# Kernel tuning notes

Measured on AMD Instinct MI355X. Metric: run time of the kernel, lower is better.

## Reference

```python
import jax, jax.numpy as jnp
import numpy as np

B, T, C, H = 2, 2048, 1024, 4
D = C // H
STRIDES = [1, 3, 7, 13]  # spiral_strides[:n_head]
SCALE = 1.0 / float(np.sqrt(D))


def _build_mask():
    """Static [H, T, T] bool mask: spiral positions intersected with causal.
    Replicates: positions = set((i+offset)%T for offset in range(-T//2, T//2, stride)),
    then keep only p <= i."""
    m = np.zeros((H, T, T), dtype=bool)
    i = np.arange(T)
    causal = (np.arange(T)[None, :] <= i[:, None])
    for h in range(H):
        s = STRIDES[h % len(STRIDES)]
        off = np.arange(-(T // 2), T // 2, s)
        pos = (i[:, None] + off[None, :]) % T  # [T, n_off]
        mh = np.zeros((T, T), dtype=bool)
        mh[np.repeat(i, len(off)), pos.ravel()] = True  # set semantics (dupes ok)
        m[h] = mh & causal
    return jnp.asarray(m)

MASK = _build_mask()  # [H, T, T]


def setup_inputs() -> dict:
    ks = jax.random.split(jax.random.key(0), 4)
    s = 0.02
    return {
        "x": jax.random.normal(ks[0], (B, T, C), jnp.float32),
        "Wqk": jax.random.normal(ks[1], (C, C), jnp.float32) * s,
        "bqk": jnp.zeros((C,), jnp.float32),
        "Wv": jax.random.normal(ks[2], (C, C), jnp.float32) * s,
        "bv": jnp.zeros((C,), jnp.float32),
        "Wo": jax.random.normal(ks[3], (C, C), jnp.float32) * s,
        "bo": jnp.zeros((C,), jnp.float32),
    }


def reference(x, Wqk, bqk, Wv, bv, Wo, bo):
    qk = x @ Wqk.T + bqk                                   # [B,T,C]; q == k in source
    q = qk.reshape(B, T, H, D).transpose(0, 2, 1, 3)       # [B,H,T,D]
    v = (x @ Wv.T + bv).reshape(B, T, H, D).transpose(0, 2, 1, 3)
    scores = jnp.einsum('bhid,bhjd->bhij', q, q) * SCALE   # [B,H,T,T]
    NEG = jnp.float32(-1e30)
    logits = jnp.where(MASK[None], scores, NEG)
    w = jax.nn.softmax(logits, axis=-1)
    # Rows with no causal spiral position stay all-zero (matches torch scatter behavior)
    w = jnp.where(MASK[None], w, jnp.float32(0.0))
    out = jnp.einsum('bhij,bhjd->bhid', w, v)              # [B,H,T,D]
    out = out.transpose(0, 2, 1, 3).reshape(B, T, C)
    return out @ Wo.T + bo
```

## Files before the change

kernel.cpp:

```cpp
#include <hip/hip_runtime.h>
#include <cstdint>
#include <cstddef>

typedef unsigned short u16;
typedef uint32_t u32;
typedef __bf16 bf16x8 __attribute__((ext_vector_type(8)));
typedef float f32x4 __attribute__((ext_vector_type(4)));
typedef float f32x16 __attribute__((ext_vector_type(16)));

typedef __attribute__((address_space(1))) void gvoid;
typedef __attribute__((address_space(3))) void lvoid;

__device__ __forceinline__ void g2l16(const void* g, void* l) {
    __builtin_amdgcn_global_load_lds((gvoid*)g, (lvoid*)l, 16, 0, 0);
}

__device__ __forceinline__ u16 f2bf(float f) {
    union { float f; uint32_t u; } v;
    v.f = f;
    uint32_t r = (v.u + 0x7FFFu + ((v.u >> 16) & 1u)) >> 16;
    return (u16)r;
}

__device__ const int T_h[24]  = {0, 1,1,1, 2,2,2,2,2,2,2, 3,3,3,3,3,3,3,3,3,3,3,3,3};
__device__ const int T_g[24]  = {0, 0,1,2, 0,1,2,3,4,5,6, 0,1,2,3,4,5,6,7,8,9,10,11,12};
__device__ const int T_qt[24] = {0, 64,86,108, 130,140,150,160,170,180,190,
                                 200,205,210,215,220,225,230,235,240,245,250,255,260};
__device__ const int T_LQ[24] = {2048, 683,683,682, 293,293,293,293,292,292,292,
                                 158,158,158,158,158,158,158,157,157,157,157,157,157};
__device__ const int T_ktB[24]= {0, 64,86,108, 140,150,160,170,180,190,130,
                                 245,250,255,260,200,205,210,215,220,225,230,235,240};
__device__ const int T_LkB[24]= {2048, 683,683,682, 293,293,293,292,292,292,293,
                                 157,157,157,157,158,158,158,158,158,158,158,157,157};
__device__ const int T_cB[24] = {1, -341,-341,-341, -146,-146,-146,-146,-146,-146,-145,
                                 -79,-79,-79,-79,-78,-78,-78,-78,-78,-78,-78,-78,-78};
__device__ const int T_ktA[24]= {0, 108,64,86, 180,190,130,140,150,160,170,
                                 215,220,225,230,235,240,245,250,255,260,200,205,210};
__device__ const int T_LkA[24]= {0, 682,683,683, 292,292,293,293,293,293,292,
                                 158,158,158,158,157,157,157,157,157,157,158,158,158};
__device__ const int T_cA[24] = {0, -342,-341,-341, -147,-147,-146,-146,-146,-146,-146,
                                 -79,-79,-79,-79,-79,-79,-79,-79,-79,-79,-78,-78,-78};
__device__ const int T_dA[24] = {0, 0,1,1, 0,0,1,1,1,1,1, 0,0,0,0,0,0,0,0,0,0,1,1,1};
__device__ const int T_nc[24] = {16, 6,6,6, 3,3,3,3,3,3,3, 2,2,2,2,2,2,2,2,2,2,2,2,2};

__device__ __forceinline__ void col_geom(int p, int c, int& ntB, int& tA0, int& nt) {
    const int LQ = T_LQ[p];
    const int Mc = c << 7;
    int mmax = Mc + 128; if (mmax > LQ) mmax = LQ; mmax -= 1;
    int jB = mmax + T_cB[p];
    if (jB < 0) jB = 0;
    if (jB > T_LkB[p]) jB = T_LkB[p];
    ntB = (jB + 31) >> 5;
    int jlo = Mc + T_cA[p]; if (jlo < 0) jlo = 0;
    int jhi = mmax + T_dA[p];
    if (jhi > T_LkA[p]) jhi = T_LkA[p];
    tA0 = jlo >> 5;
    int ntA = 0;
    if (jhi > jlo) ntA = ((jhi + 31) >> 5) - tA0;
    nt = ntB + ntA;
}

__device__ __forceinline__ u16* partO_addr(u16* lo, u16* hi, int slot) {
    return (slot < 128) ? (lo + (size_t)slot * 32768) : (hi + (size_t)(slot - 128) * 32768);
}
__device__ __forceinline__ const u16* partO_addr_c(const u16* lo, const u16* hi, int slot) {
    return (slot < 128) ? (lo + (size_t)slot * 32768) : (hi + (size_t)(slot - 128) * 32768);
}

__global__ __launch_bounds__(256)
void cvt_kernel(const float* __restrict__ x, const float* __restrict__ wqk,
                const float* __restrict__ wv, const float* __restrict__ wo,
                u16* __restrict__ out) {
    int i = (blockIdx.x * 256 + threadIdx.x) * 4;
    const float* src;
    int off;
    if (i < 4194304)      { src = x;   off = 0; }
    else if (i < 5242880) { src = wqk; off = 4194304; }
    else if (i < 6291456) { src = wv;  off = 5242880; }
    else                  { src = wo;  off = 6291456; }
    float4 v = *(const float4*)(src + (i - off));
    ushort4 o;
    o.x = f2bf(v.x); o.y = f2bf(v.y); o.z = f2bf(v.z); o.w = f2bf(v.w);
    *(ushort4*)(out + i) = o;
}

__global__ __launch_bounds__(256, 3)
void gemm_qkv(const u16* __restrict__ A, const u16* __restrict__ Bq, const u16* __restrict__ Bv,
              const float* __restrict__ bq, const float* __restrict__ bv,
              u16* __restrict__ qkb, u16* __restrict__ vb) {
    __shared__ __align__(16) u16 As[2][4096], Bqs[2][2048], Bvs[2][2048];
    const int bid = blockIdx.x;
    const int xcd = bid & 7, slot = bid >> 3;
    const int m0 = ((xcd >> 1) * 8 + (slot & 7)) * 128;
    const int n0 = ((xcd & 1) * 8 + (slot >> 3)) * 64;
    const int t = threadIdx.x;
    const int lane = t & 63;
    const int wid = t >> 6;
    const int wr = wid >> 1, wc = wid & 1;
    const int l15 = lane & 15, l4 = lane >> 4;

    f32x4 aq[4][2] = {}, av[4][2] = {};

    auto stage = [&](int buf, int kt) {
        const int kbase = kt * 32;
#pragma unroll
        for (int c2 = 0; c2 < 2; ++c2) {
            const int pp = c2 * 4096 + t * 16;
            g2l16(A + (size_t)(m0 + (pp >> 6)) * 1024 + kbase + ((pp & 63) >> 1), (char*)As[buf] + pp);
        }
        const int pb = t * 16;
        const int rb = pb >> 6, kb = (pb & 63) >> 1;
        g2l16(Bq + (size_t)(n0 + rb) * 1024 + kbase + kb, (char*)Bqs[buf] + pb);
        g2l16(Bv + (size_t)(n0 + rb) * 1024 + kbase + kb, (char*)Bvs[buf] + pb);
    };

    stage(0, 0);
    asm volatile("s_waitcnt vmcnt(0)" ::: "memory");
    __syncthreads();

    int cur = 0;
    for (int kt = 0; kt < 32; ++kt) {
        if (kt + 1 < 32) stage(cur ^ 1, kt + 1);
        bf16x8 af[4], bfq[2], bfv[2];
#pragma unroll
        for (int mi = 0; mi < 4; ++mi)
            af[mi] = *(const bf16x8*)((const char*)As[cur] + (wr * 64 + mi * 16 + l15) * 64 + l4 * 16);
#pragma unroll
        for (int ni = 0; ni < 2; ++ni) {
            bfq[ni] = *(const bf16x8*)((const char*)Bqs[cur] + (wc * 32 + ni * 16 + l15) * 64 + l4 * 16);
            bfv[ni] = *(const bf16x8*)((const char*)Bvs[cur] + (wc * 32 + ni * 16 + l15) * 64 + l4 * 16);
        }
        __builtin_amdgcn_s_setprio(1);
#pragma unroll
        for (int mi = 0; mi < 4; ++mi)
#pragma unroll
            for (int ni = 0; ni < 2; ++ni) {
                aq[mi][ni] = __builtin_amdgcn_mfma_f32_16x16x32_bf16(af[mi], bfq[ni], aq[mi][ni], 0, 0, 0);
                av[mi][ni] = __builtin_amdgcn_mfma_f32_16x16x32_bf16(af[mi], bfv[ni], av[mi][ni], 0, 0, 0);
            }
        __builtin_amdgcn_s_setprio(0);
        asm volatile("s_waitcnt vmcnt(0)" ::: "memory");
        __syncthreads();
        cur ^= 1;
    }

    const int mbase = m0 + wr * 64 + l4 * 4;
    const int nbase = n0 + wc * 32 + l15;
#pragma unroll
    for (int ni = 0; ni < 2; ++ni) {
        const int n = nbase + ni * 16;
        const float bq_ = bq[n];
        const float bv_ = bv[n];
#pragma unroll
        for (int mi = 0; mi < 4; ++mi) {
            const int mrow = mbase + mi * 16;
#pragma unroll
            for (int r = 0; r < 4; ++r) {
                qkb[(size_t)(mrow + r) * 1024 + n] = f2bf(aq[mi][ni][r] + bq_);
                vb [(size_t)(mrow + r) * 1024 + n] = f2bf(av[mi][ni][r] + bv_);
            }
        }
    }
}

__device__ __forceinline__ void tile_decode(int tt, int& h, int& cls, int& jt, int& LK) {
    if (tt < 64)       { h = 0; cls = 0;               jt = tt;              LK = 2048; }
    else if (tt < 130) { h = 1; cls = (tt - 64) / 22;  jt = (tt - 64) % 22;  LK = (cls < 2) ? 683 : 682; }
    else if (tt < 200) { h = 2; cls = (tt - 130) / 10; jt = (tt - 130) % 10; LK = (cls < 4) ? 293 : 292; }
    else               { h = 3; cls = (tt - 200) / 5;  jt = (tt - 200) % 5;  LK = (cls < 7) ? 158 : 157; }
}

__global__ __launch_bounds__(256)
void repack_kv(const u16* __restrict__ qkb, const u16* __restrict__ vb,
               u16* __restrict__ kpack, u16* __restrict__ vpack) {
    __shared__ __align__(16) unsigned char sm[32768];
    const int bid = blockIdx.x;
    const int b = bid & 1;
    const int tt = bid >> 1;
    int h, cls, jt, LK;
    tile_decode(tt, h, cls, jt, LK);
    const int s = (h == 0) ? 1 : (h == 1) ? 3 : (h == 2) ? 7 : 13;
    const int j0 = jt * 32;
    int nval = LK - j0; if (nval > 32) nval = 32;
    const int t = threadIdx.x;

#pragma unroll
    for (int i2 = 0; i2 < 4; ++i2) {
        const int p = i2 * 4096 + t * 16;
        const int j = p >> 9;
        const int cb = (p & 511) ^ ((j & 31) << 4);
        const int jj = (j < nval) ? j : (nval - 1);
        const size_t gofs = (size_t)((b * 2048 + cls + (j0 + jj) * s) * 1024 + h * 256) + (cb >> 1);
        g2l16(qkb + gofs, sm + p);
        g2l16(vb  + gofs, sm + 16384 + p);
    }
    asm volatile("s_waitcnt vmcnt(0)" ::: "memory");
    __syncthreads();
    if (nval < 32) {
        const int pb = 16384 + nval * 512;
        for (int off = pb + t * 16; off < 32768; off += 4096) {
            uint4 z; z.x = 0; z.y = 0; z.z = 0; z.w = 0;
            *(uint4*)(sm + off) = z;
        }
        __syncthreads();
    }
    const size_t tb = (size_t)(b * 265 + tt) * 8192;
#pragma unroll
    for (int i2 = 0; i2 < 4; ++i2) {
        const int o = (i2 * 256 + t) * 8;
        const int dc = o >> 9;
        const int idx = (o >> 3) & 63;
        const int j = idx & 31;
        const int d0 = dc * 16 + (idx >> 5) * 8;
        const uint4 pk = *(const uint4*)(sm + j * 512 + ((d0 * 2) ^ ((j & 31) << 4)));
        *(uint4*)(kpack + tb + o) = pk;
    }
#pragma unroll
    for (int i2 = 0; i2 < 4; ++i2) {
        const int o = (i2 * 256 + t) * 8;
        const int slot2 = o >> 9;
        const int idx = (o >> 3) & 63;
        const int jb = (slot2 >> 3) * 16 + (idx >> 5) * 8;
        const int d = (slot2 & 7) * 32 + (idx & 31);
        u32 wpk[4];
#pragma unroll
        for (int e2 = 0; e2 < 4; ++e2) {
            const int j1 = jb + e2 * 2, j2 = j1 + 1;
            const u16 a0 = *(const u16*)(sm + 16384 + j1 * 512 + (((d >> 3) ^ (j1 & 31)) << 4) + (d & 7) * 2);
            const u16 a1 = *(const u16*)(sm + 16384 + j2 * 512 + (((d >> 3) ^ (j2 & 31)) << 4) + (d & 7) * 2);
            wpk[e2] = (u32)a0 | ((u32)a1 << 16);
        }
        uint4 pk; pk.x = wpk[0]; pk.y = wpk[1]; pk.z = wpk[2]; pk.w = wpk[3];
        *(uint4*)(vpack + tb + o) = pk;
    }
}

__global__ __launch_bounds__(256, 2)
void attn_kernel(const u16* __restrict__ kpack, const u16* __restrict__ vpack,
                 u16* __restrict__ attnb, u16* __restrict__ partLo, u16* __restrict__ partHi,
                 float* __restrict__ mlbuf) {
    __shared__ __align__(16) unsigned char sm[65536];
    static constexpr int CGc[24] = {0,16,22,28,34,37,40,43,46,49,52,55,
                                    57,59,61,63,65,67,69,71,73,75,77,79};
    static constexpr int EXc[24] = {0,56,64,72,80,82,84,86,88,90,92,94,
                                    94,94,94,94,94,94,94,94,94,94,94,94};
    static constexpr int Tpc[24] = {72,14,14,14,5,5,5,5,5,5,5,2,2,2,2,2,2,2,2,2,2,2,2,2};

    const int bid = blockIdx.x;
    const int xcd = bid & 7, slot = bid >> 3;
    const int b = xcd & 1, quad = xcd >> 1;
    int hsel, hcb;
    if (quad == 0) {
        if (slot >= 37) return;
        hsel = 0; hcb = slot;
    } else if (quad == 1) {
        if (slot < 35)      { hsel = 0; hcb = 37 + slot; }
        else if (slot < 43) { hsel = 3; hcb = slot - 35; }
        else return;
    } else if (quad == 2) {
        if (slot >= 42) return;
        hsel = 1; hcb = slot;
    } else {
        if (slot < 35)      { hsel = 2; hcb = slot; }
        else if (slot < 53) { hsel = 3; hcb = 8 + (slot - 35); }
        else return;
    }
    int p = (hsel == 0) ? 0 : (hsel == 1) ? 1 : (hsel == 2) ? 4 : 11;
    int rb = hcb;
    while (rb >= Tpc[p]) { rb -= Tpc[p]; ++p; }
    int colg = CGc[p], exb = EXc[p];

    const int LQ = T_LQ[p];
    const int cB = T_cB[p], cA = T_cA[p], dA = T_dA[p];
    const int LKB = T_LkB[p], LKA = T_LkA[p];
    const int ktB = T_ktB[p], ktA = T_ktA[p];
    const int h = T_h[p], g = T_g[p], nc = T_nc[p], qt0 = T_qt[p];
    const int s = (h == 0) ? 1 : (h == 1) ? 3 : (h == 2) ? 7 : 13;

    int col = 0, chunk = 0, ntB = 0, tA0 = 0, nt = 0;
    for (int c = nc - 1; c >= 0; --c) {
        const int Mc = c << 7;
        int mmax = Mc + 128; if (mmax > LQ) mmax = LQ; mmax -= 1;
        int jB = mmax + cB; if (jB < 0) jB = 0; if (jB > LKB) jB = LKB;
        const int nb = (jB + 31) >> 5;
        int jlo = Mc + cA; if (jlo < 0) jlo = 0;
        int jhi = mmax + dA; if (jhi > LKA) jhi = LKA;
        const int ta = jlo >> 5;
        const int na = (jhi > jlo) ? (((jhi + 31) >> 5) - ta) : 0;
        const int n = nb + na;
        const int nch2 = (n + 7) >> 3;
        if (rb < nch2) { col = c; chunk = rb; ntB = nb; tA0 = ta; nt = n; break; }
        rb -= nch2; ++colg; exb += nch2 - 1;
    }
    const int nch = (nt + 7) >> 3;
    const int PBi = b * 265;

    const int t = threadIdx.x;
    const int w = t >> 6;
    const int l = t & 63;
    const int l31 = l & 31, h5 = l >> 5;
    const int m = (col << 7) + (w << 5) + l31;
    const float c2 = 0.09016844f;
    const int lane16 = l * 16;

    bf16x8 qf[16];
    {
        const u16* qb = kpack + (size_t)(PBi + qt0 + col * 4 + w) * 8192 + l * 8;
#pragma unroll
        for (int dc = 0; dc < 16; ++dc)
            qf[dc] = *(const bf16x8*)(qb + dc * 512);
    }

    auto tileof = [&](int tv) -> int {
        return (tv < ntB) ? (ktB + tv) : (ktA + tA0 + (tv - ntB));
    };
    auto stage = [&](int tv, int buf) {
        const size_t tb = (size_t)(PBi + tileof(tv)) * 8192;
        unsigned char* Kd = sm + buf * 32768;
        unsigned char* Vd = Kd + 16384;
#pragma unroll
        for (int i2 = 0; i2 < 4; ++i2) {
            const int off = i2 * 4096 + t * 16;
            g2l16(kpack + tb + (off >> 1), Kd + off);
            g2l16(vpack + tb + (off >> 1), Vd + off);
        }
    };

    const int tt0 = chunk * 8;
    int tt1 = tt0 + 8; if (tt1 > nt) tt1 = nt;

    f32x16 o[8] = {};
    float mrun = -3.0e38f, lrun = 0.0f;

    stage(tt0, 0);
    asm volatile("s_waitcnt vmcnt(0)" ::: "memory");
    __syncthreads();

    int buf = 0;
    for (int tv = tt0; tv < tt1; ++tv) {
        if (tv + 1 < tt1) stage(tv + 1, buf ^ 1);

        int j0, lo, hi;
        if (tv < ntB) { j0 = tv << 5; lo = -100000; hi = cB; }
        else { const int ta = tA0 + tv - ntB; j0 = ta << 5; lo = cA; hi = dA; }

        const unsigned char* Kb = sm + buf * 32768;
        const unsigned char* Vb = Kb + 16384;

        f32x16 sacc = {};
        __builtin_amdgcn_s_setprio(1);
#pragma unroll
        for (int dc = 0; dc < 16; ++dc) {
            const bf16x8 kf = *(const bf16x8*)(Kb + dc * 1024 + lane16);
            sacc = __builtin_amdgcn_mfma_f32_32x32x16_bf16(kf, qf[dc], sacc, 0, 0, 0);
        }
        __builtin_amdgcn_s_setprio(0);

        const int ebase = j0 - m;
        float tmax = -3.0e38f;
#pragma unroll
        for (int r = 0; r < 16; ++r) {
            const int km = (r & 3) + 8 * (r >> 2) + 4 * h5;
            const int e = ebase + km;
            const bool ok = (e >= lo) && (e < hi);
            sacc[r] = ok ? sacc[r] : -3.0e38f;
            tmax = fmaxf(tmax, sacc[r]);
        }
        tmax = fmaxf(tmax, __shfl_xor(tmax, 32, 64));
        if (!__all(tmax <= mrun + 8.0f)) {
            const float mnew = fmaxf(mrun, tmax);
            const float fsc = __builtin_amdgcn_exp2f((mrun - mnew) * c2);
            lrun *= fsc;
#pragma unroll
            for (int ch = 0; ch < 8; ++ch)
#pragma unroll
                for (int r = 0; r < 16; ++r)
                    o[ch][r] *= fsc;
            mrun = mnew;
        }
        float psum = 0.0f;
#pragma unroll
        for (int r = 0; r < 16; ++r) {
            const float pv = (sacc[r] > -1.0e37f) ? __builtin_amdgcn_exp2f((sacc[r] - mrun) * c2) : 0.0f;
            sacc[r] = pv;
            psum += pv;
        }
        lrun += psum;

        uint32_t w0, w1, w2, w3, w4, w5, w6, w7;
        asm("v_cvt_pk_bf16_f32 %0,%1,%2" : "=v"(w0) : "v"(sacc[0]),  "v"(sacc[1]));
        asm("v_cvt_pk_bf16_f32 %0,%1,%2" : "=v"(w1) : "v"(sacc[2]),  "v"(sacc[3]));
        asm("v_cvt_pk_bf16_f32 %0,%1,%2" : "=v"(w2) : "v"(sacc[4]),  "v"(sacc[5]));
        asm("v_cvt_pk_bf16_f32 %0,%1,%2" : "=v"(w3) : "v"(sacc[6]),  "v"(sacc[7]));
        asm("v_cvt_pk_bf16_f32 %0,%1,%2" : "=v"(w4) : "v"(sacc[8]),  "v"(sacc[9]));
        asm("v_cvt_pk_bf16_f32 %0,%1,%2" : "=v"(w5) : "v"(sacc[10]), "v"(sacc[11]));
        asm("v_cvt_pk_bf16_f32 %0,%1,%2" : "=v"(w6) : "v"(sacc[12]), "v"(sacc[13]));
        asm("v_cvt_pk_bf16_f32 %0,%1,%2" : "=v"(w7) : "v"(sacc[14]), "v"(sacc[15]));
        asm("v_permlane32_swap_b32 %0, %1" : "+v"(w0), "+v"(w2));
        asm("v_permlane32_swap_b32 %0, %1" : "+v"(w1), "+v"(w3));
        asm("v_permlane32_swap_b32 %0, %1" : "+v"(w4), "+v"(w6));
        asm("v_permlane32_swap_b32 %0, %1" : "+v"(w5), "+v"(w7));
        union { uint32_t u[4]; bf16x8 v; } p0u, p1u;
        p0u.u[0] = w0; p0u.u[1] = w1; p0u.u[2] = w2; p0u.u[3] = w3;
        p1u.u[0] = w4; p1u.u[1] = w5; p1u.u[2] = w6; p1u.u[3] = w7;

        __builtin_amdgcn_s_setprio(1);
#pragma unroll
        for (int kk = 0; kk < 2; ++kk) {
            const bf16x8 pf = kk ? p1u.v : p0u.v;
#pragma unroll
            for (int ch = 0; ch < 8; ++ch) {
                const bf16x8 vf = *(const bf16x8*)(Vb + (kk * 8 + ch) * 1024 + lane16);
                o[ch] = __builtin_amdgcn_mfma_f32_32x32x16_bf16(vf, pf, o[ch], 0, 0, 0);
            }
        }
        __builtin_amdgcn_s_setprio(0);

        asm volatile("s_waitcnt vmcnt(0)" ::: "memory");
        __syncthreads();
        buf ^= 1;
    }

    lrun += __shfl_xor(lrun, 32, 64);

    float scale = 1.0f;
    u16* ab;
    const int qm = (w << 5) + l31;
    if (nch == 1) {
        scale = (lrun > 0.0f) ? 1.0f / lrun : 0.0f;
        ab = attnb + ((size_t)(b * 2048 + g + m * s)) * 1024 + h * 256;
    } else {
        if (h5 == 0 && m < LQ) {
            const int colid = b * 81 + colg;
            mlbuf[(size_t)((colid * 8 + chunk) * 256) + qm * 2]     = mrun;
            mlbuf[(size_t)((colid * 8 + chunk) * 256) + qm * 2 + 1] = lrun;
        }
        if (chunk == 0)
            ab = attnb + ((size_t)(b * 2048 + g + m * s)) * 1024 + h * 256;
        else
            ab = partO_addr(partLo, partHi, b * 94 + exb + chunk - 1) + (size_t)qm * 256;
    }

    if (m < LQ) {
#pragma unroll
        for (int ch = 0; ch < 8; ++ch) {
#pragma unroll
            for (int g2 = 0; g2 < 4; ++g2) {
                ushort4 wv4;
                wv4.x = f2bf(o[ch][g2 * 4 + 0] * scale);
                wv4.y = f2bf(o[ch][g2 * 4 + 1] * scale);
                wv4.z = f2bf(o[ch][g2 * 4 + 2] * scale);
                wv4.w = f2bf(o[ch][g2 * 4 + 3] * scale);
                *(ushort4*)(ab + ch * 32 + 8 * g2 + 4 * h5) = wv4;
            }
        }
    }
}

__global__ __launch_bounds__(256)
void combine_kernel(const u16* __restrict__ partLo, const u16* __restrict__ partHi,
                    const float* __restrict__ mlbuf, u16* __restrict__ attnb) {
    static constexpr int MCc[24] = {0,14,18,22,26,28,30,32,34,36,38,40,
                                    40,40,40,40,40,40,40,40,40,40,40,40};
    static constexpr int CGc[24] = {0,16,22,28,34,37,40,43,46,49,52,55,
                                    57,59,61,63,65,67,69,71,73,75,77,79};
    static constexpr int EXc[24] = {0,56,64,72,80,82,84,86,88,90,92,94,
                                    94,94,94,94,94,94,94,94,94,94,94,94};
    const int b = blockIdx.x & 1;
    int rb = blockIdx.x >> 1;
    int p = 0, base = 0, colg = 0, exb = 0;
#pragma unroll
    for (int i = 1; i < 24; ++i)
        if (rb >= MCc[i]) { p = i; base = MCc[i]; colg = CGc[i]; exb = EXc[i]; }
    rb -= base;

    int col = 0, nch = 0;
    for (int c = T_nc[p] - 1; c >= 0; --c) {
        int nb, ta, n;
        col_geom(p, c, nb, ta, n);
        const int nc2 = (n + 7) >> 3;
        if (nc2 > 1) {
            if (rb == 0) { col = c; nch = nc2; break; }
            --rb;
        }
        ++colg; exb += nc2 - 1;
    }
    const int h = T_h[p], g = T_g[p];
    const int s = (h == 0) ? 1 : (h == 1) ? 3 : (h == 2) ? 7 : 13;
    const int LQ = T_LQ[p];
    const int colid = b * 81 + colg;
    const float c2 = 0.09016844f;

    const int t = threadIdx.x;
    const int q = t >> 1, dpart = (t & 1) * 128;
    const int m = (col << 7) + q;

    float mj[8], lj[8];
#pragma unroll
    for (int j5 = 0; j5 < 8; ++j5) {
        if (j5 < nch) {
            mj[j5] = mlbuf[(size_t)((colid * 8 + j5) * 256) + q * 2];
            lj[j5] = mlbuf[(size_t)((colid * 8 + j5) * 256) + q * 2 + 1];
        } else { mj[j5] = -3.0e38f; lj[j5] = 0.0f; }
    }
    float M = -3.0e38f;
#pragma unroll
    for (int j5 = 0; j5 < 8; ++j5) if (j5 < nch) M = fmaxf(M, mj[j5]);
    float L = 0.0f, al[8];
#pragma unroll
    for (int j5 = 0; j5 < 8; ++j5) {
        al[j5] = (j5 < nch) ? __builtin_amdgcn_exp2f((mj[j5] - M) * c2) : 0.0f;
        L += lj[j5] * al[j5];
    }
    const float inv = (L > 0.0f) ? 1.0f / L : 0.0f;
#pragma unroll
    for (int j5 = 0; j5 < 8; ++j5) al[j5] *= inv;

    u16* dst = attnb + ((size_t)(b * 2048 + g + m * s)) * 1024 + h * 256 + dpart;

    for (int ss = 0; ss < 4; ++ss) {
        float acc32[32];
#pragma unroll
        for (int e = 0; e < 32; ++e) acc32[e] = 0.0f;
#pragma unroll
        for (int j5 = 0; j5 < 8; ++j5) {
            if (j5 >= nch) continue;
            const u16* src = (j5 == 0)
                ? (dst + ss * 32)
                : (partO_addr_c(partLo, partHi, b * 94 + exb + j5 - 1) + (size_t)q * 256 + dpart + ss * 32);
            const float sc = al[j5];
#pragma unroll
            for (int w4 = 0; w4 < 4; ++w4) {
                const uint4 pk = *(const uint4*)(src + w4 * 8);
                const u32 ww[4] = { pk.x, pk.y, pk.z, pk.w };
#pragma unroll
                for (int e = 0; e < 4; ++e) {
                    union { u32 u; float f; } lo2, hi2;
                    lo2.u = ww[e] << 16;
                    hi2.u = ww[e] & 0xffff0000u;
                    acc32[w4 * 8 + e * 2]     += sc * lo2.f;
                    acc32[w4 * 8 + e * 2 + 1] += sc * hi2.f;
                }
            }
        }
        if (m < LQ) {
#pragma unroll
            for (int w4 = 0; w4 < 4; ++w4) {
                uint4 pk;
                pk.x = (u32)f2bf(acc32[w4 * 8 + 0]) | ((u32)f2bf(acc32[w4 * 8 + 1]) << 16);
                pk.y = (u32)f2bf(acc32[w4 * 8 + 2]) | ((u32)f2bf(acc32[w4 * 8 + 3]) << 16);
                pk.z = (u32)f2bf(acc32[w4 * 8 + 4]) | ((u32)f2bf(acc32[w4 * 8 + 5]) << 16);
                pk.w = (u32)f2bf(acc32[w4 * 8 + 6]) | ((u32)f2bf(acc32[w4 * 8 + 7]) << 16);
                *(uint4*)(dst + ss * 32 + w4 * 8) = pk;
            }
        }
    }
}

__global__ __launch_bounds__(256, 3)
void gemm_out(const u16* __restrict__ A, const u16* __restrict__ Bw,
              const float* __restrict__ bias, float* __restrict__ outp) {
    __shared__ __align__(16) u16 As[2][4096], Bs[2][2048];
    const int bid = blockIdx.x;
    const int xcd = bid & 7, slot = bid >> 3;
    const int m0 = (xcd * 4 + (slot & 3)) * 128;
    const int n0 = (slot >> 2) * 64;
    const int t = threadIdx.x;
    const int lane = t & 63;
    const int wid = t >> 6;
    const int wr = wid >> 1, wc = wid & 1;
    const int l15 = lane & 15, l4 = lane >> 4;

    f32x4 acc[4][2] = {};

    auto stage = [&](int buf, int kt) {
        const int kbase = kt * 32;
#pragma unroll
        for (int c2 = 0; c2 < 2; ++c2) {
            const int pp = c2 * 4096 + t * 16;
            g2l16(A + (size_t)(m0 + (pp >> 6)) * 1024 + kbase + ((pp & 63) >> 1), (char*)As[buf] + pp);
        }
        const int pb = t * 16;
        g2l16(Bw + (size_t)(n0 + (pb >> 6)) * 1024 + kbase + ((pb & 63) >> 1), (char*)Bs[buf] + pb);
    };

    stage(0, 0);
    asm volatile("s_waitcnt vmcnt(0)" ::: "memory");
    __syncthreads();

    int cur = 0;
    for (int kt = 0; kt < 32; ++kt) {
        if (kt + 1 < 32) stage(cur ^ 1, kt + 1);
        bf16x8 af[4], bfr[2];
#pragma unroll
        for (int mi = 0; mi < 4; ++mi)
            af[mi] = *(const bf16x8*)((const char*)As[cur] + (wr * 64 + mi * 16 + l15) * 64 + l4 * 16);
#pragma unroll
        for (int ni = 0; ni < 2; ++ni)
            bfr[ni] = *(const bf16x8*)((const char*)Bs[cur] + (wc * 32 + ni * 16 + l15) * 64 + l4 * 16);
        __builtin_amdgcn_s_setprio(1);
#pragma unroll
        for (int mi = 0; mi < 4; ++mi)
#pragma unroll
            for (int ni = 0; ni < 2; ++ni)
                acc[mi][ni] = __builtin_amdgcn_mfma_f32_16x16x32_bf16(af[mi], bfr[ni], acc[mi][ni], 0, 0, 0);
        __builtin_amdgcn_s_setprio(0);
        asm volatile("s_waitcnt vmcnt(0)" ::: "memory");
        __syncthreads();
        cur ^= 1;
    }

    const int mbase = m0 + wr * 64 + l4 * 4;
    const int nbase = n0 + wc * 32 + l15;
#pragma unroll
    for (int ni = 0; ni < 2; ++ni) {
        const int n = nbase + ni * 16;
        const float bv = bias[n];
#pragma unroll
        for (int mi = 0; mi < 4; ++mi) {
            const int mrow = mbase + mi * 16;
#pragma unroll
            for (int r = 0; r < 4; ++r)
                outp[(size_t)(mrow + r) * 1024 + n] = acc[mi][ni][r] + bv;
        }
    }
}

extern "C" void kernel_launch(void* const* d_in, const int* in_sizes, int n_in,
                              void* d_out, int out_size, void* d_ws, size_t ws_size,
                              hipStream_t stream) {
    const float* x   = (const float*)d_in[0];
    const float* Wqk = (const float*)d_in[1];
    const float* bqk = (const float*)d_in[2];
    const float* Wv  = (const float*)d_in[3];
    const float* bv  = (const float*)d_in[4];
    const float* Wo  = (const float*)d_in[5];
    const float* bo  = (const float*)d_in[6];
    float* out = (float*)d_out;

    u16* ws     = (u16*)d_ws;
    u16* xb     = ws;
    u16* wqkb   = ws + 4194304;
    u16* wvb    = ws + 5242880;
    u16* wob    = ws + 6291456;
    u16* qkb    = ws + 7340032;
    u16* vb     = ws + 11534336;
    u16* kpack  = ws + 15728640;
    u16* vpack  = ws + 20070400;
    u16* attnb  = ws;
    u16* partLo = ws + 7340032;
    u16* partHi = ws + 4194304;
    float* mlbuf = (float*)d_out;

    cvt_kernel<<<7168, 256, 0, stream>>>(x, Wqk, Wv, Wo, ws);
    gemm_qkv<<<512, 256, 0, stream>>>(xb, wqkb, wvb, bqk, bv, qkb, vb);
    repack_kv<<<530, 256, 0, stream>>>(qkb, vb, kpack, vpack);
    attn_kernel<<<424, 256, 0, stream>>>(kpack, vpack, attnb, partLo, partHi, mlbuf);
    combine_kernel<<<80, 256, 0, stream>>>(partLo, partHi, mlbuf, attnb);
    gemm_out<<<512, 256, 0, stream>>>(attnb, wob, bo, out);
}
```

Baseline: 121.3 us.

## Double K-tile depth to 64 with XOR-swizzled LDS layout in projection GEMMs

```diff
diff --git a/kernel.cpp b/kernel.cpp
--- a/kernel.cpp
+++ b/kernel.cpp
@@ -84,11 +84,11 @@
     *(ushort4*)(out + i) = o;
 }
 
-__global__ __launch_bounds__(256, 3)
+__global__ __launch_bounds__(256, 2)
 void gemm_qkv(const u16* __restrict__ A, const u16* __restrict__ Bq, const u16* __restrict__ Bv,
               const float* __restrict__ bq, const float* __restrict__ bv,
               u16* __restrict__ qkb, u16* __restrict__ vb) {
-    __shared__ __align__(16) u16 As[2][4096], Bqs[2][2048], Bvs[2][2048];
+    __shared__ __align__(16) u16 As[2][8192], Bqs[2][4096], Bvs[2][4096];
     const int bid = blockIdx.x;
     const int xcd = bid & 7, slot = bid >> 3;
     const int m0 = ((xcd >> 1) * 8 + (slot & 7)) * 128;
@@ -102,16 +102,23 @@
     f32x4 aq[4][2] = {}, av[4][2] = {};
 
     auto stage = [&](int buf, int kt) {
-        const int kbase = kt * 32;
+        const int kbase = kt * 64;
+#pragma unroll
+        for (int c2 = 0; c2 < 4; ++c2) {
+            const int p = c2 * 4096 + t * 16;
+            const int row = p >> 7;
+            const int cs = ((p >> 4) & 7) ^ (row & 7);
+            g2l16(A + (size_t)(m0 + row) * 1024 + kbase + cs * 8, (char*)As[buf] + p);
+        }
 #pragma unroll
         for (int c2 = 0; c2 < 2; ++c2) {
-            const int pp = c2 * 4096 + t * 16;
-            g2l16(A + (size_t)(m0 + (pp >> 6)) * 1024 + kbase + ((pp & 63) >> 1), (char*)As[buf] + pp);
-        }
-        const int pb = t * 16;
-        const int rb = pb >> 6, kb = (pb & 63) >> 1;
-        g2l16(Bq + (size_t)(n0 + rb) * 1024 + kbase + kb, (char*)Bqs[buf] + pb);
-        g2l16(Bv + (size_t)(n0 + rb) * 1024 + kbase + kb, (char*)Bvs[buf] + pb);
+            const int p = c2 * 4096 + t * 16;
+            const int row = p >> 7;
+            const int cs = ((p >> 4) & 7) ^ (row & 7);
+            const size_t so = (size_t)(n0 + row) * 1024 + kbase + cs * 8;
+            g2l16(Bq + so, (char*)Bqs[buf] + p);
+            g2l16(Bv + so, (char*)Bvs[buf] + p);
+        }
     };
 
     stage(0, 0);
@@ -119,26 +126,33 @@
     __syncthreads();
 
     int cur = 0;
-    for (int kt = 0; kt < 32; ++kt) {
-        if (kt + 1 < 32) stage(cur ^ 1, kt + 1);
-        bf16x8 af[4], bfq[2], bfv[2];
-#pragma unroll
-        for (int mi = 0; mi < 4; ++mi)
-            af[mi] = *(const bf16x8*)((const char*)As[cur] + (wr * 64 + mi * 16 + l15) * 64 + l4 * 16);
-#pragma unroll
-        for (int ni = 0; ni < 2; ++ni) {
-            bfq[ni] = *(const bf16x8*)((const char*)Bqs[cur] + (wc * 32 + ni * 16 + l15) * 64 + l4 * 16);
-            bfv[ni] = *(const bf16x8*)((const char*)Bvs[cur] + (wc * 32 + ni * 16 + l15) * 64 + l4 * 16);
-        }
-        __builtin_amdgcn_s_setprio(1);
-#pragma unroll
-        for (int mi = 0; mi < 4; ++mi)
+    for (int kt = 0; kt < 16; ++kt) {
+        if (kt + 1 < 16) stage(cur ^ 1, kt + 1);
+#pragma unroll
+        for (int kk = 0; kk < 2; ++kk) {
+            bf16x8 af[4], bfq[2], bfv[2];
+#pragma unroll
+            for (int mi = 0; mi < 4; ++mi) {
+                const int row = wr * 64 + mi * 16 + l15;
+                af[mi] = *(const bf16x8*)((const char*)As[cur] + row * 128 + (((kk * 4 + l4) ^ (row & 7)) << 4));
+            }
 #pragma unroll
             for (int ni = 0; ni < 2; ++ni) {
-                aq[mi][ni] = __builtin_amdgcn_mfma_f32_16x16x32_bf16(af[mi], bfq[ni], aq[mi][ni], 0, 0, 0);
-                av[mi][ni] = __builtin_amdgcn_mfma_f32_16x16x32_bf16(af[mi], bfv[ni], av[mi][ni], 0, 0, 0);
-            }
-        __builtin_amdgcn_s_setprio(0);
+                const int row = wc * 32 + ni * 16 + l15;
+                const int co = row * 128 + (((kk * 4 + l4) ^ (row & 7)) << 4);
+                bfq[ni] = *(const bf16x8*)((const char*)Bqs[cur] + co);
+                bfv[ni] = *(const bf16x8*)((const char*)Bvs[cur] + co);
+            }
+            __builtin_amdgcn_s_setprio(1);
+#pragma unroll
+            for (int mi = 0; mi < 4; ++mi)
+#pragma unroll
+                for (int ni = 0; ni < 2; ++ni) {
+                    aq[mi][ni] = __builtin_amdgcn_mfma_f32_16x16x32_bf16(af[mi], bfq[ni], aq[mi][ni], 0, 0, 0);
+                    av[mi][ni] = __builtin_amdgcn_mfma_f32_16x16x32_bf16(af[mi], bfv[ni], av[mi][ni], 0, 0, 0);
+                }
+            __builtin_amdgcn_s_setprio(0);
+        }
         asm volatile("s_waitcnt vmcnt(0)" ::: "memory");
         __syncthreads();
         cur ^= 1;
@@ -557,10 +571,10 @@
     }
 }
 
-__global__ __launch_bounds__(256, 3)
+__global__ __launch_bounds__(256, 2)
 void gemm_out(const u16* __restrict__ A, const u16* __restrict__ Bw,
               const float* __restrict__ bias, float* __restrict__ outp) {
-    __shared__ __align__(16) u16 As[2][4096], Bs[2][2048];
+    __shared__ __align__(16) u16 As[2][8192], Bs[2][4096];
     const int bid = blockIdx.x;
     const int xcd = bid & 7, slot = bid >> 3;
     const int m0 = (xcd * 4 + (slot & 3)) * 128;
@@ -574,14 +588,21 @@
     f32x4 acc[4][2] = {};
 
     auto stage = [&](int buf, int kt) {
-        const int kbase = kt * 32;
+        const int kbase = kt * 64;
+#pragma unroll
+        for (int c2 = 0; c2 < 4; ++c2) {
+            const int p = c2 * 4096 + t * 16;
+            const int row = p >> 7;
+            const int cs = ((p >> 4) & 7) ^ (row & 7);
+            g2l16(A + (size_t)(m0 + row) * 1024 + kbase + cs * 8, (char*)As[buf] + p);
+        }
 #pragma unroll
         for (int c2 = 0; c2 < 2; ++c2) {
-            const int pp = c2 * 4096 + t * 16;
-            g2l16(A + (size_t)(m0 + (pp >> 6)) * 1024 + kbase + ((pp & 63) >> 1), (char*)As[buf] + pp);
-        }
-        const int pb = t * 16;
-        g2l16(Bw + (size_t)(n0 + (pb >> 6)) * 1024 + kbase + ((pb & 63) >> 1), (char*)Bs[buf] + pb);
+            const int p = c2 * 4096 + t * 16;
+            const int row = p >> 7;
+            const int cs = ((p >> 4) & 7) ^ (row & 7);
+            g2l16(Bw + (size_t)(n0 + row) * 1024 + kbase + cs * 8, (char*)Bs[buf] + p);
+        }
     };
 
     stage(0, 0);
@@ -589,22 +610,29 @@
     __syncthreads();
 
     int cur = 0;
-    for (int kt = 0; kt < 32; ++kt) {
-        if (kt + 1 < 32) stage(cur ^ 1, kt + 1);
-        bf16x8 af[4], bfr[2];
-#pragma unroll
-        for (int mi = 0; mi < 4; ++mi)
-            af[mi] = *(const bf16x8*)((const char*)As[cur] + (wr * 64 + mi * 16 + l15) * 64 + l4 * 16);
-#pragma unroll
-        for (int ni = 0; ni < 2; ++ni)
-            bfr[ni] = *(const bf16x8*)((const char*)Bs[cur] + (wc * 32 + ni * 16 + l15) * 64 + l4 * 16);
-        __builtin_amdgcn_s_setprio(1);
-#pragma unroll
-        for (int mi = 0; mi < 4; ++mi)
-#pragma unroll
-            for (int ni = 0; ni < 2; ++ni)
-                acc[mi][ni] = __builtin_amdgcn_mfma_f32_16x16x32_bf16(af[mi], bfr[ni], acc[mi][ni], 0, 0, 0);
-        __builtin_amdgcn_s_setprio(0);
+    for (int kt = 0; kt < 16; ++kt) {
+        if (kt + 1 < 16) stage(cur ^ 1, kt + 1);
+#pragma unroll
+        for (int kk = 0; kk < 2; ++kk) {
+            bf16x8 af[4], bfr[2];
+#pragma unroll
+            for (int mi = 0; mi < 4; ++mi) {
+                const int row = wr * 64 + mi * 16 + l15;
+                af[mi] = *(const bf16x8*)((const char*)As[cur] + row * 128 + (((kk * 4 + l4) ^ (row & 7)) << 4));
+            }
+#pragma unroll
+            for (int ni = 0; ni < 2; ++ni) {
+                const int row = wc * 32 + ni * 16 + l15;
+                bfr[ni] = *(const bf16x8*)((const char*)Bs[cur] + row * 128 + (((kk * 4 + l4) ^ (row & 7)) << 4));
+            }
+            __builtin_amdgcn_s_setprio(1);
+#pragma unroll
+            for (int mi = 0; mi < 4; ++mi)
+#pragma unroll
+                for (int ni = 0; ni < 2; ++ni)
+                    acc[mi][ni] = __builtin_amdgcn_mfma_f32_16x16x32_bf16(af[mi], bfr[ni], acc[mi][ni], 0, 0, 0);
+            __builtin_amdgcn_s_setprio(0);
+        }
         asm volatile("s_waitcnt vmcnt(0)" ::: "memory");
         __syncthreads();
         cur ^= 1;
```

Result: faster. 112.3 us (-7.5%).
